# Kernel tuning notes

Hardware: AMD Instinct MI355X
Metric: run time of the kernel (lower is better)

## Reference

```python
import jax, jax.numpy as jnp
import numpy as np

D_MODEL = 1024
D_HEAD = 64

def setup_inputs() -> dict:
    key = jax.random.key(0)
    ks = jax.random.split(key, 7)
    s = 1.0 / np.sqrt(D_MODEL)
    x = jax.random.normal(ks[0], (4, 4096, D_MODEL), dtype=jnp.float32)
    Wq = jax.random.uniform(ks[1], (D_MODEL, D_HEAD), jnp.float32, -s, s)
    bq = jax.random.uniform(ks[2], (D_HEAD,), jnp.float32, -s, s)
    Wk = jax.random.uniform(ks[3], (D_MODEL, D_HEAD), jnp.float32, -s, s)
    bk = jax.random.uniform(ks[4], (D_HEAD,), jnp.float32, -s, s)
    Wv = jax.random.uniform(ks[5], (D_MODEL, D_HEAD), jnp.float32, -s, s)
    bv = jax.random.uniform(ks[6], (D_HEAD,), jnp.float32, -s, s)
    return {"x": x, "Wq": Wq, "bq": bq, "Wk": Wk, "bk": bk, "Wv": Wv, "bv": bv}

def reference(x, Wq, bq, Wk, bk, Wv, bv):
    # x: [b, s, d_model] -> Q,K,V: [b, s, d_head]
    Q = jnp.einsum('bsd,dh->bsh', x, Wq) + bq
    K = jnp.einsum('bsd,dh->bsh', x, Wk) + bk
    V = jnp.einsum('bsd,dh->bsh', x, Wv) + bv
    scale = 1.0 / jnp.sqrt(jnp.asarray(D_HEAD, x.dtype))
    scores = jnp.einsum('bqh,bkh->bqk', Q, K) * scale  # [b, s, s]
    attn = jax.nn.softmax(scores, axis=-1)
    return jnp.einsum('bqk,bkh->bqh', attn, V)  # [b, s, d_head]
```

## Files before the change

### kernel.cpp

```cpp
#include <hip/hip_runtime.h>

typedef __bf16 bf16x8 __attribute__((ext_vector_type(8)));
typedef __bf16 bf16x4 __attribute__((ext_vector_type(4)));
typedef float f32x4 __attribute__((ext_vector_type(4)));
typedef unsigned short u16x8 __attribute__((ext_vector_type(8)));

union FragU { u16x8 u; bf16x8 b; };
union PackU { bf16x4 v; unsigned long long q; };

__device__ __forceinline__ unsigned short bfbits(float f) {
  __bf16 h = (__bf16)f;
  union { __bf16 h; unsigned short s; } cv; cv.h = h;
  return cv.s;
}

#define MFMA16(a, b, c) __builtin_amdgcn_mfma_f32_16x16x32_bf16((a), (b), (c), 0, 0, 0)

#define QSCALE 0.18033688011112042f

__global__ __launch_bounds__(256) void wt_kernel(
    const float* __restrict__ Wq, const float* __restrict__ Wk, const float* __restrict__ Wv,
    unsigned short* __restrict__ WF)
{
  const int m = blockIdx.x >> 5;
  const int c = blockIdx.x & 31;
  const float* W = (m == 0) ? Wq : ((m == 1) ? Wk : Wv);
  const int t = threadIdx.x >> 6;
  const int lane = threadIdx.x & 63;
  const int l15 = lane & 15;
  const int g = lane >> 4;
  unsigned short* dst = WF + ((((size_t)m * 32 + c) * 4 + t) * 64 + lane) * 8;
#pragma unroll
  for (int e = 0; e < 8; ++e)
    dst[e] = bfbits(W[(size_t)(32 * c + 8 * g + e) * 64 + (16 * t + l15)]);
}

__global__ __launch_bounds__(256, 1) void proj_kernel(
    const float* __restrict__ x, const unsigned short* __restrict__ WF,
    const float* __restrict__ bq, const float* __restrict__ bk, const float* __restrict__ bv,
    unsigned short* __restrict__ Qb, unsigned short* __restrict__ KF,
    unsigned short* __restrict__ VF)
{
  const int tid = threadIdx.x;
  const int lane = tid & 63;
  const int wid = tid >> 6;
  const int l15 = lane & 15;
  const int g = lane >> 4;
  const int row0 = blockIdx.x * 64 + wid * 16;

  f32x4 accQ[4], accK[4], accV[4];
  const f32x4 zero = {0.f, 0.f, 0.f, 0.f};
#pragma unroll
  for (int i = 0; i < 4; ++i) { accQ[i] = zero; accK[i] = zero; accV[i] = zero; }

  const float* xrow = x + (size_t)(row0 + l15) * 1024;

  f32x4 xx0[4], xx1[4];
  bf16x8 wq[2][4], wk[2][4], wv[2][4];

#define PLDX(XB, C) { xx0[XB] = *(const f32x4*)(xrow + 32 * (C) + 8 * g); \
                      xx1[XB] = *(const f32x4*)(xrow + 32 * (C) + 8 * g + 4); }
#define PLDW(WS, C) { _Pragma("unroll") for (int t = 0; t < 4; ++t) { \
    wq[WS][t] = *(const bf16x8*)(WF + ((((size_t)0 * 32 + (C)) * 4 + t) * 64 + lane) * 8); \
    wk[WS][t] = *(const bf16x8*)(WF + ((((size_t)1 * 32 + (C)) * 4 + t) * 64 + lane) * 8); \
    wv[WS][t] = *(const bf16x8*)(WF + ((((size_t)2 * 32 + (C)) * 4 + t) * 64 + lane) * 8); } }
#define PHALF(XB, WS, CXN, CWN) { \
    FragU xf; \
    _Pragma("unroll") for (int i = 0; i < 4; ++i) { \
      xf.b[i] = (__bf16)xx0[XB][i]; xf.b[4 + i] = (__bf16)xx1[XB][i]; } \
    if ((CXN) < 32) PLDX(XB, CXN); \
    _Pragma("unroll") for (int t = 0; t < 4; ++t) { \
      accQ[t] = MFMA16(xf.b, wq[WS][t], accQ[t]); \
      accK[t] = MFMA16(xf.b, wk[WS][t], accK[t]); \
      accV[t] = MFMA16(wv[WS][t], xf.b, accV[t]); } \
    if ((CWN) < 32) PLDW(WS, CWN); }

  PLDX(0, 0) PLDX(1, 1) PLDX(2, 2) PLDX(3, 3)
  PLDW(0, 0) PLDW(1, 1)

#pragma unroll 1
  for (int c = 0; c < 32; c += 4) {
    PHALF(0, 0, c + 4, c + 2)
    PHALF(1, 1, c + 5, c + 3)
    PHALF(2, 0, c + 6, c + 4)
    PHALF(3, 1, c + 7, c + 5)
  }

  const int b = blockIdx.x >> 6;
  const int kt = blockIdx.x & 63;
  const int q0 = row0 & 4095;
  unsigned short* Qbase = Qb + (size_t)b * 4096 * 64;
#pragma unroll
  for (int t = 0; t < 4; ++t) {
    const int h = 16 * t + l15;
    const float bqv = bq[h];
#pragma unroll
    for (int r = 0; r < 4; ++r)
      Qbase[(size_t)(q0 + 4 * g + r) * 64 + h] = bfbits((accQ[t][r] + bqv) * QSCALE);
  }
  unsigned short* KFb = KF + ((size_t)b * 64 + kt) * 4096;
  unsigned short* VFb = VF + ((size_t)b * 64 + kt) * 4096;
#pragma unroll
  for (int t = 0; t < 4; ++t) {
    const int h = 16 * t + l15;
    const float bkv = bk[h];
#pragma unroll
    for (int r = 0; r < 4; ++r) {
      KFb[(size_t)((wid * 2 + (t >> 1)) * 64 + (t & 1) * 32 + (l15 >> 3) * 16 + 4 * g + r) * 8 +
          (l15 & 7)] = bfbits(accK[t][r] + bkv);
      const int hv = 16 * t + 4 * g + r;
      VFb[(size_t)((t * 2 + (wid >> 1)) * 64 + (wid & 1) * 32 + (l15 >> 3) * 16 + 4 * g + r) * 8 +
          (l15 & 7)] = bfbits(accV[t][r] + bv[hv]);
    }
  }
}

__global__ __launch_bounds__(256, 2) void flash_kernel(
    const unsigned short* __restrict__ Qb, const unsigned short* __restrict__ KF,
    const unsigned short* __restrict__ VF, float* __restrict__ out)
{
  __shared__ __align__(16) unsigned char lds[36864];
  const int tid = threadIdx.x;
  const int lane = tid & 63;
  const int w = tid >> 6;
  const int l15 = lane & 15;
  const int g = lane >> 4;
  const int bid = blockIdx.x;
  const int xcd = bid & 7;
  const int b = xcd >> 1;
  const int qt = (bid >> 3) * 2 + (xcd & 1);
  const int q0 = qt * 32;

  const unsigned short* Qp = Qb + (size_t)b * 4096 * 64;
  const unsigned short* KFb = KF + (size_t)b * 262144;
  const unsigned short* VFb = VF + (size_t)b * 262144;

  const bf16x8 qfA0 = *(const bf16x8*)(Qp + (size_t)(q0 + l15) * 64 + 8 * g);
  const bf16x8 qfA1 = *(const bf16x8*)(Qp + (size_t)(q0 + l15) * 64 + 32 + 8 * g);
  const bf16x8 qfB0 = *(const bf16x8*)(Qp + (size_t)(q0 + 16 + l15) * 64 + 8 * g);
  const bf16x8 qfB1 = *(const bf16x8*)(Qp + (size_t)(q0 + 16 + l15) * 64 + 32 + 8 * g);

  f32x4 O_A[4], O_B[4];
  const f32x4 zero = {0.f, 0.f, 0.f, 0.f};
#pragma unroll
  for (int i = 0; i < 4; ++i) { O_A[i] = zero; O_B[i] = zero; }
  float mA = -INFINITY, lA = 0.f, mB = -INFINITY, lB = 0.f;
  unsigned short* PwA = (unsigned short*)lds + (w * 2 + 0) * 1152;
  unsigned short* PwB = (unsigned short*)lds + (w * 2 + 1) * 1152;

#define SM_HALF(S, mvar, lvar, OA, PW) { \
  float mt = fmaxf(fmaxf(S[0][0], S[0][1]), fmaxf(S[0][2], S[0][3])); \
  _Pragma("unroll") for (int t = 1; t < 4; ++t) \
    _Pragma("unroll") for (int r = 0; r < 4; ++r) mt = fmaxf(mt, S[t][r]); \
  mt = fmaxf(mt, __shfl_xor(mt, 16)); \
  mt = fmaxf(mt, __shfl_xor(mt, 32)); \
  if (!__all(mt <= mvar + 8.0f)) { \
    const float mnew = fmaxf(mvar, mt); \
    const float alpha = __builtin_amdgcn_exp2f(mvar - mnew); \
    mvar = mnew; lvar *= alpha; \
    _Pragma("unroll") for (int r = 0; r < 4; ++r) { \
      const float ar = __shfl(alpha, 4 * g + r); \
      OA[0][r] *= ar; OA[1][r] *= ar; OA[2][r] *= ar; OA[3][r] *= ar; } \
  } \
  float ps = 0.f; \
  _Pragma("unroll") for (int t = 0; t < 4; ++t) { \
    const float p0 = __builtin_amdgcn_exp2f(S[t][0] - mvar); \
    const float p1 = __builtin_amdgcn_exp2f(S[t][1] - mvar); \
    const float p2 = __builtin_amdgcn_exp2f(S[t][2] - mvar); \
    const float p3 = __builtin_amdgcn_exp2f(S[t][3] - mvar); \
    ps += (p0 + p1) + (p2 + p3); \
    PackU pk_; pk_.v[0] = (__bf16)p0; pk_.v[1] = (__bf16)p1; \
    pk_.v[2] = (__bf16)p2; pk_.v[3] = (__bf16)p3; \
    *(unsigned long long*)((PW) + l15 * 72 + 16 * t + 4 * g) = pk_.q; } \
  ps += __shfl_xor(ps, 16); \
  ps += __shfl_xor(ps, 32); \
  lvar += ps; }

#pragma unroll 1
  for (int kt = w; kt < 64; kt += 4) {
    const unsigned short* Kt = KFb + kt * 4096;
    const unsigned short* Vt = VFb + kt * 4096;
    bf16x8 kf[8], vf[8];
#pragma unroll
    for (int j = 0; j < 8; ++j) kf[j] = *(const bf16x8*)(Kt + (j * 64 + lane) * 8);
#pragma unroll
    for (int j = 0; j < 8; ++j) vf[j] = *(const bf16x8*)(Vt + (j * 64 + lane) * 8);
    f32x4 S_A[4], S_B[4];
#pragma unroll
    for (int t = 0; t < 4; ++t) {
      S_A[t] = zero;
      S_A[t] = MFMA16(kf[2 * t], qfA0, S_A[t]);
      S_A[t] = MFMA16(kf[2 * t + 1], qfA1, S_A[t]);
      S_B[t] = zero;
      S_B[t] = MFMA16(kf[2 * t], qfB0, S_B[t]);
      S_B[t] = MFMA16(kf[2 * t + 1], qfB1, S_B[t]);
    }
    SM_HALF(S_A, mA, lA, O_A, PwA)
    SM_HALF(S_B, mB, lB, O_B, PwB)
#pragma unroll
    for (int s = 0; s < 2; ++s) {
      const bf16x8 paA = *(const bf16x8*)(PwA + l15 * 72 + 32 * s + 8 * g);
      const bf16x8 paB = *(const bf16x8*)(PwB + l15 * 72 + 32 * s + 8 * g);
#pragma unroll
      for (int nt = 0; nt < 4; ++nt) {
        O_A[nt] = MFMA16(paA, vf[2 * nt + s], O_A[nt]);
        O_B[nt] = MFMA16(paB, vf[2 * nt + s], O_B[nt]);
      }
    }
  }

  __syncthreads();
  float* O_l = (float*)lds;
  float* mlp = (float*)(lds + 34816);
#pragma unroll
  for (int nt = 0; nt < 4; ++nt)
#pragma unroll
    for (int r = 0; r < 4; ++r) {
      O_l[((w * 2 + 0) * 16 + 4 * g + r) * 68 + 16 * nt + l15] = O_A[nt][r];
      O_l[((w * 2 + 1) * 16 + 4 * g + r) * 68 + 16 * nt + l15] = O_B[nt][r];
    }
  if (g == 0) {
    mlp[((w * 2 + 0) * 16 + l15) * 2] = mA; mlp[((w * 2 + 0) * 16 + l15) * 2 + 1] = lA;
    mlp[((w * 2 + 1) * 16 + l15) * 2] = mB; mlp[((w * 2 + 1) * 16 + l15) * 2 + 1] = lB;
  }
  __syncthreads();

  const int q = tid >> 3;
  const int h0 = (tid & 7) * 8;
  const int qh = q >> 4, qr = q & 15;
  float M = -INFINITY;
#pragma unroll
  for (int s = 0; s < 4; ++s) M = fmaxf(M, mlp[((s * 2 + qh) * 16 + qr) * 2]);
  float L = 0.f;
  f32x4 a0 = zero, a1 = zero;
#pragma unroll
  for (int s = 0; s < 4; ++s) {
    const int rowi = (s * 2 + qh) * 16 + qr;
    const float wgt = __builtin_amdgcn_exp2f(mlp[rowi * 2] - M);
    L += wgt * mlp[rowi * 2 + 1];
    const f32x4 o0 = *(const f32x4*)&O_l[rowi * 68 + h0];
    const f32x4 o1 = *(const f32x4*)&O_l[rowi * 68 + h0 + 4];
#pragma unroll
    for (int i = 0; i < 4; ++i) { a0[i] += wgt * o0[i]; a1[i] += wgt * o1[i]; }
  }
  const float inv = 1.0f / L;
  float* ob = out + ((size_t)b * 4096 + qt * 32 + q) * 64 + h0;
  f32x4 r0 = {a0[0] * inv, a0[1] * inv, a0[2] * inv, a0[3] * inv};
  f32x4 r1 = {a1[0] * inv, a1[1] * inv, a1[2] * inv, a1[3] * inv};
  *(f32x4*)ob = r0;
  *(f32x4*)(ob + 4) = r1;
}

extern "C" void kernel_launch(void* const* d_in, const int* in_sizes, int n_in,
                              void* d_out, int out_size, void* d_ws, size_t ws_size,
                              hipStream_t stream) {
  const float* x  = (const float*)d_in[0];
  const float* Wq = (const float*)d_in[1];
  const float* bq = (const float*)d_in[2];
  const float* Wk = (const float*)d_in[3];
  const float* bk = (const float*)d_in[4];
  const float* Wv = (const float*)d_in[5];
  const float* bv = (const float*)d_in[6];

  char* ws = (char*)d_ws;
  unsigned short* WF = (unsigned short*)ws;
  unsigned short* Qb = (unsigned short*)(ws + (512u << 10));
  unsigned short* KF = (unsigned short*)(ws + (512u << 10) + (2u << 20));
  unsigned short* VF = (unsigned short*)(ws + (512u << 10) + (4u << 20));
  float* out = (float*)d_out;

  hipLaunchKernelGGL(wt_kernel,    dim3(96),  dim3(256), 0, stream, Wq, Wk, Wv, WF);
  hipLaunchKernelGGL(proj_kernel,  dim3(256), dim3(256), 0, stream, x, WF, bq, bk, bv, Qb, KF, VF);
  hipLaunchKernelGGL(flash_kernel, dim3(512), dim3(256), 0, stream, Qb, KF, VF, out);
}
```

Baseline: 61.34 us.

## Split projection K-dimension across waves with LDS reduction, quadruple grid

The projection kernel now gives each block 16 rows instead of 64, and its four waves each handle one quarter of the 1024-wide reduction dimension. Partial Q/K/V accumulators are reduced through shared memory, and three waves write out Q, K and V respectively. The grid grows from 256 to 1024 blocks to fill more CUs and hide memory latency better. In exchange it adds a 48KB LDS buffer, a barrier and a reduction step, and each block reloads all the weights for only 16 rows.

```diff
diff --git a/kernel.cpp b/kernel.cpp
--- a/kernel.cpp
+++ b/kernel.cpp
@@ -35,18 +35,19 @@
     dst[e] = bfbits(W[(size_t)(32 * c + 8 * g + e) * 64 + (16 * t + l15)]);
 }
 
-__global__ __launch_bounds__(256, 1) void proj_kernel(
+__global__ __launch_bounds__(256, 3) void proj_kernel(
     const float* __restrict__ x, const unsigned short* __restrict__ WF,
     const float* __restrict__ bq, const float* __restrict__ bk, const float* __restrict__ bv,
     unsigned short* __restrict__ Qb, unsigned short* __restrict__ KF,
     unsigned short* __restrict__ VF)
 {
+  __shared__ f32x4 part[4][3][4][64];
   const int tid = threadIdx.x;
   const int lane = tid & 63;
-  const int wid = tid >> 6;
+  const int w = tid >> 6;
   const int l15 = lane & 15;
   const int g = lane >> 4;
-  const int row0 = blockIdx.x * 64 + wid * 16;
+  const int row0 = blockIdx.x * 16;
 
   f32x4 accQ[4], accK[4], accV[4];
   const f32x4 zero = {0.f, 0.f, 0.f, 0.f};
@@ -68,49 +69,83 @@
     FragU xf; \
     _Pragma("unroll") for (int i = 0; i < 4; ++i) { \
       xf.b[i] = (__bf16)xx0[XB][i]; xf.b[4 + i] = (__bf16)xx1[XB][i]; } \
-    if ((CXN) < 32) PLDX(XB, CXN); \
+    if ((CXN) < cend) PLDX(XB, CXN); \
     _Pragma("unroll") for (int t = 0; t < 4; ++t) { \
       accQ[t] = MFMA16(xf.b, wq[WS][t], accQ[t]); \
       accK[t] = MFMA16(xf.b, wk[WS][t], accK[t]); \
       accV[t] = MFMA16(wv[WS][t], xf.b, accV[t]); } \
-    if ((CWN) < 32) PLDW(WS, CWN); }
-
-  PLDX(0, 0) PLDX(1, 1) PLDX(2, 2) PLDX(3, 3)
-  PLDW(0, 0) PLDW(1, 1)
+    if ((CWN) < cend) PLDW(WS, CWN); }
+
+  const int c0 = w * 8;
+  const int cend = c0 + 8;
+  PLDX(0, c0) PLDX(1, c0 + 1) PLDX(2, c0 + 2) PLDX(3, c0 + 3)
+  PLDW(0, c0) PLDW(1, c0 + 1)
 
 #pragma unroll 1
-  for (int c = 0; c < 32; c += 4) {
+  for (int c = c0; c < cend; c += 4) {
     PHALF(0, 0, c + 4, c + 2)
     PHALF(1, 1, c + 5, c + 3)
     PHALF(2, 0, c + 6, c + 4)
     PHALF(3, 1, c + 7, c + 5)
   }
 
-  const int b = blockIdx.x >> 6;
-  const int kt = blockIdx.x & 63;
+#pragma unroll
+  for (int t = 0; t < 4; ++t) {
+    part[w][0][t][lane] = accQ[t];
+    part[w][1][t][lane] = accK[t];
+    part[w][2][t][lane] = accV[t];
+  }
+  __syncthreads();
+  if (w == 3) return;
+
+  const int m = w;
+  f32x4 sum[4];
+#pragma unroll
+  for (int t = 0; t < 4; ++t) {
+    f32x4 s = part[0][m][t][lane];
+#pragma unroll
+    for (int ws = 1; ws < 4; ++ws) {
+      const f32x4 p = part[ws][m][t][lane];
+#pragma unroll
+      for (int i = 0; i < 4; ++i) s[i] += p[i];
+    }
+    sum[t] = s;
+  }
+
+  const int b = blockIdx.x >> 8;
   const int q0 = row0 & 4095;
-  unsigned short* Qbase = Qb + (size_t)b * 4096 * 64;
-#pragma unroll
-  for (int t = 0; t < 4; ++t) {
-    const int h = 16 * t + l15;
-    const float bqv = bq[h];
-#pragma unroll
-    for (int r = 0; r < 4; ++r)
-      Qbase[(size_t)(q0 + 4 * g + r) * 64 + h] = bfbits((accQ[t][r] + bqv) * QSCALE);
-  }
-  unsigned short* KFb = KF + ((size_t)b * 64 + kt) * 4096;
-  unsigned short* VFb = VF + ((size_t)b * 64 + kt) * 4096;
-#pragma unroll
-  for (int t = 0; t < 4; ++t) {
-    const int h = 16 * t + l15;
-    const float bkv = bk[h];
-#pragma unroll
-    for (int r = 0; r < 4; ++r) {
-      KFb[(size_t)((wid * 2 + (t >> 1)) * 64 + (t & 1) * 32 + (l15 >> 3) * 16 + 4 * g + r) * 8 +
-          (l15 & 7)] = bfbits(accK[t][r] + bkv);
-      const int hv = 16 * t + 4 * g + r;
-      VFb[(size_t)((t * 2 + (wid >> 1)) * 64 + (wid & 1) * 32 + (l15 >> 3) * 16 + 4 * g + r) * 8 +
-          (l15 & 7)] = bfbits(accV[t][r] + bv[hv]);
+  const int kt = (blockIdx.x & 255) >> 2;
+  const int r16 = blockIdx.x & 3;
+  if (m == 0) {
+    unsigned short* Qbase = Qb + (size_t)b * 4096 * 64;
+#pragma unroll
+    for (int t = 0; t < 4; ++t) {
+      const float bqv = bq[16 * t + l15];
+#pragma unroll
+      for (int r = 0; r < 4; ++r)
+        Qbase[(size_t)(q0 + 4 * g + r) * 64 + 16 * t + l15] =
+            bfbits((sum[t][r] + bqv) * QSCALE);
+    }
+  } else if (m == 1) {
+    unsigned short* KFb = KF + ((size_t)b * 64 + kt) * 4096;
+#pragma unroll
+    for (int t = 0; t < 4; ++t) {
+      const float bkv = bk[16 * t + l15];
+#pragma unroll
+      for (int r = 0; r < 4; ++r)
+        KFb[(size_t)((r16 * 2 + (t >> 1)) * 64 + (t & 1) * 32 + (l15 >> 3) * 16 + 4 * g + r) * 8 +
+            (l15 & 7)] = bfbits(sum[t][r] + bkv);
+    }
+  } else {
+    unsigned short* VFb = VF + ((size_t)b * 64 + kt) * 4096;
+#pragma unroll
+    for (int t = 0; t < 4; ++t) {
+#pragma unroll
+      for (int r = 0; r < 4; ++r) {
+        const int hv = 16 * t + 4 * g + r;
+        VFb[(size_t)((t * 2 + (r16 >> 1)) * 64 + (r16 & 1) * 32 + (l15 >> 3) * 16 + 4 * g + r) * 8 +
+            (l15 & 7)] = bfbits(sum[t][r] + bv[hv]);
+      }
     }
   }
 }
@@ -269,7 +304,7 @@
   unsigned short* VF = (unsigned short*)(ws + (512u << 10) + (4u << 20));
   float* out = (float*)d_out;
 
-  hipLaunchKernelGGL(wt_kernel,    dim3(96),  dim3(256), 0, stream, Wq, Wk, Wv, WF);
-  hipLaunchKernelGGL(proj_kernel,  dim3(256), dim3(256), 0, stream, x, WF, bq, bk, bv, Qb, KF, VF);
-  hipLaunchKernelGGL(flash_kernel, dim3(512), dim3(256), 0, stream, Qb, KF, VF, out);
-}
+  hipLaunchKernelGGL(wt_kernel,    dim3(96),   dim3(256), 0, stream, Wq, Wk, Wv, WF);
+  hipLaunchKernelGGL(proj_kernel,  dim3(1024), dim3(256), 0, stream, x, WF, bq, bk, bv, Qb, KF, VF);
+  hipLaunchKernelGGL(flash_kernel, dim3(512),  dim3(256), 0, stream, Qb, KF, VF, out);
+}
```

Result: slower. 85.88 us (+40.0%).

## Split QKV projection into separate per-matrix blocks for more parallelism

Applied to the files above, without the earlier changes.

The projection kernel now launches three times as many blocks. Each block computes only one of Q, K or V for its 64-row tile, with a single accumulator set and a smaller weight buffer. Launch bounds go from 1 to 4 blocks per SM, so more blocks run at once on the 256-CU device, where previously only 256 blocks ran. The cost is that x is read from memory three times instead of once, which adds traffic on a bandwidth-heavy kernel that reads 64MB of fp32 input.

```diff
diff --git a/kernel.cpp b/kernel.cpp
--- a/kernel.cpp
+++ b/kernel.cpp
@@ -35,82 +35,101 @@
     dst[e] = bfbits(W[(size_t)(32 * c + 8 * g + e) * 64 + (16 * t + l15)]);
 }
 
-__global__ __launch_bounds__(256, 1) void proj_kernel(
+__global__ __launch_bounds__(256, 4) void proj_kernel(
     const float* __restrict__ x, const unsigned short* __restrict__ WF,
     const float* __restrict__ bq, const float* __restrict__ bk, const float* __restrict__ bv,
     unsigned short* __restrict__ Qb, unsigned short* __restrict__ KF,
     unsigned short* __restrict__ VF)
 {
+  const int bid = blockIdx.x;
+  const int m = bid >> 8;
+  const int rb = bid & 255;
   const int tid = threadIdx.x;
   const int lane = tid & 63;
   const int wid = tid >> 6;
   const int l15 = lane & 15;
   const int g = lane >> 4;
-  const int row0 = blockIdx.x * 64 + wid * 16;
-
-  f32x4 accQ[4], accK[4], accV[4];
+  const int row0 = rb * 64 + wid * 16;
+
+  f32x4 acc[4];
   const f32x4 zero = {0.f, 0.f, 0.f, 0.f};
 #pragma unroll
-  for (int i = 0; i < 4; ++i) { accQ[i] = zero; accK[i] = zero; accV[i] = zero; }
+  for (int i = 0; i < 4; ++i) acc[i] = zero;
 
   const float* xrow = x + (size_t)(row0 + l15) * 1024;
+  const unsigned short* Wm = WF + (size_t)m * 65536;
 
   f32x4 xx0[4], xx1[4];
-  bf16x8 wq[2][4], wk[2][4], wv[2][4];
-
-#define PLDX(XB, C) { xx0[XB] = *(const f32x4*)(xrow + 32 * (C) + 8 * g); \
+  bf16x8 wf[2][4];
+
+#define QLDX(XB, C) { xx0[XB] = *(const f32x4*)(xrow + 32 * (C) + 8 * g); \
                       xx1[XB] = *(const f32x4*)(xrow + 32 * (C) + 8 * g + 4); }
-#define PLDW(WS, C) { _Pragma("unroll") for (int t = 0; t < 4; ++t) { \
-    wq[WS][t] = *(const bf16x8*)(WF + ((((size_t)0 * 32 + (C)) * 4 + t) * 64 + lane) * 8); \
-    wk[WS][t] = *(const bf16x8*)(WF + ((((size_t)1 * 32 + (C)) * 4 + t) * 64 + lane) * 8); \
-    wv[WS][t] = *(const bf16x8*)(WF + ((((size_t)2 * 32 + (C)) * 4 + t) * 64 + lane) * 8); } }
-#define PHALF(XB, WS, CXN, CWN) { \
+#define QLDW(WS, C) { _Pragma("unroll") for (int t = 0; t < 4; ++t) \
+    wf[WS][t] = *(const bf16x8*)(Wm + (((size_t)(C) * 4 + t) * 64 + lane) * 8); }
+#define QHALF(XB, WS, CXN, CWN, ISV) { \
     FragU xf; \
     _Pragma("unroll") for (int i = 0; i < 4; ++i) { \
       xf.b[i] = (__bf16)xx0[XB][i]; xf.b[4 + i] = (__bf16)xx1[XB][i]; } \
-    if ((CXN) < 32) PLDX(XB, CXN); \
+    if ((CXN) < 32) QLDX(XB, CXN); \
     _Pragma("unroll") for (int t = 0; t < 4; ++t) { \
-      accQ[t] = MFMA16(xf.b, wq[WS][t], accQ[t]); \
-      accK[t] = MFMA16(xf.b, wk[WS][t], accK[t]); \
-      accV[t] = MFMA16(wv[WS][t], xf.b, accV[t]); } \
-    if ((CWN) < 32) PLDW(WS, CWN); }
-
-  PLDX(0, 0) PLDX(1, 1) PLDX(2, 2) PLDX(3, 3)
-  PLDW(0, 0) PLDW(1, 1)
-
+      if (ISV) acc[t] = MFMA16(wf[WS][t], xf.b, acc[t]); \
+      else     acc[t] = MFMA16(xf.b, wf[WS][t], acc[t]); } \
+    if ((CWN) < 32) QLDW(WS, CWN); }
+
+  QLDX(0, 0) QLDX(1, 1) QLDX(2, 2) QLDX(3, 3)
+  QLDW(0, 0) QLDW(1, 1)
+
+  if (m == 2) {
 #pragma unroll 1
-  for (int c = 0; c < 32; c += 4) {
-    PHALF(0, 0, c + 4, c + 2)
-    PHALF(1, 1, c + 5, c + 3)
-    PHALF(2, 0, c + 6, c + 4)
-    PHALF(3, 1, c + 7, c + 5)
-  }
-
-  const int b = blockIdx.x >> 6;
-  const int kt = blockIdx.x & 63;
+    for (int c = 0; c < 32; c += 4) {
+      QHALF(0, 0, c + 4, c + 2, 1)
+      QHALF(1, 1, c + 5, c + 3, 1)
+      QHALF(2, 0, c + 6, c + 4, 1)
+      QHALF(3, 1, c + 7, c + 5, 1)
+    }
+  } else {
+#pragma unroll 1
+    for (int c = 0; c < 32; c += 4) {
+      QHALF(0, 0, c + 4, c + 2, 0)
+      QHALF(1, 1, c + 5, c + 3, 0)
+      QHALF(2, 0, c + 6, c + 4, 0)
+      QHALF(3, 1, c + 7, c + 5, 0)
+    }
+  }
+
+  const int b = rb >> 6;
+  const int kt = rb & 63;
   const int q0 = row0 & 4095;
-  unsigned short* Qbase = Qb + (size_t)b * 4096 * 64;
-#pragma unroll
-  for (int t = 0; t < 4; ++t) {
-    const int h = 16 * t + l15;
-    const float bqv = bq[h];
-#pragma unroll
-    for (int r = 0; r < 4; ++r)
-      Qbase[(size_t)(q0 + 4 * g + r) * 64 + h] = bfbits((accQ[t][r] + bqv) * QSCALE);
-  }
-  unsigned short* KFb = KF + ((size_t)b * 64 + kt) * 4096;
-  unsigned short* VFb = VF + ((size_t)b * 64 + kt) * 4096;
-#pragma unroll
-  for (int t = 0; t < 4; ++t) {
-    const int h = 16 * t + l15;
-    const float bkv = bk[h];
-#pragma unroll
-    for (int r = 0; r < 4; ++r) {
-      KFb[(size_t)((wid * 2 + (t >> 1)) * 64 + (t & 1) * 32 + (l15 >> 3) * 16 + 4 * g + r) * 8 +
-          (l15 & 7)] = bfbits(accK[t][r] + bkv);
-      const int hv = 16 * t + 4 * g + r;
-      VFb[(size_t)((t * 2 + (wid >> 1)) * 64 + (wid & 1) * 32 + (l15 >> 3) * 16 + 4 * g + r) * 8 +
-          (l15 & 7)] = bfbits(accV[t][r] + bv[hv]);
+  if (m == 0) {
+    unsigned short* Qbase = Qb + (size_t)b * 4096 * 64;
+#pragma unroll
+    for (int t = 0; t < 4; ++t) {
+      const float bqv = bq[16 * t + l15];
+#pragma unroll
+      for (int r = 0; r < 4; ++r)
+        Qbase[(size_t)(q0 + 4 * g + r) * 64 + 16 * t + l15] =
+            bfbits((acc[t][r] + bqv) * QSCALE);
+    }
+  } else if (m == 1) {
+    unsigned short* KFb = KF + ((size_t)b * 64 + kt) * 4096;
+#pragma unroll
+    for (int t = 0; t < 4; ++t) {
+      const float bkv = bk[16 * t + l15];
+#pragma unroll
+      for (int r = 0; r < 4; ++r)
+        KFb[(size_t)((wid * 2 + (t >> 1)) * 64 + (t & 1) * 32 + (l15 >> 3) * 16 + 4 * g + r) * 8 +
+            (l15 & 7)] = bfbits(acc[t][r] + bkv);
+    }
+  } else {
+    unsigned short* VFb = VF + ((size_t)b * 64 + kt) * 4096;
+#pragma unroll
+    for (int t = 0; t < 4; ++t) {
+#pragma unroll
+      for (int r = 0; r < 4; ++r) {
+        const int hv = 16 * t + 4 * g + r;
+        VFb[(size_t)((t * 2 + (wid >> 1)) * 64 + (wid & 1) * 32 + (l15 >> 3) * 16 + 4 * g + r) * 8 +
+            (l15 & 7)] = bfbits(acc[t][r] + bv[hv]);
+      }
     }
   }
 }
@@ -270,6 +289,6 @@
   float* out = (float*)d_out;
 
   hipLaunchKernelGGL(wt_kernel,    dim3(96),  dim3(256), 0, stream, Wq, Wk, Wv, WF);
-  hipLaunchKernelGGL(proj_kernel,  dim3(256), dim3(256), 0, stream, x, WF, bq, bk, bv, Qb, KF, VF);
+  hipLaunchKernelGGL(proj_kernel,  dim3(768), dim3(256), 0, stream, x, WF, bq, bk, bv, Qb, KF, VF);
   hipLaunchKernelGGL(flash_kernel, dim3(512), dim3(256), 0, stream, Qb, KF, VF, out);
 }
```

New measurement: 81.56 us. 33.0% more time.

## Stage x tiles through swizzled LDS with coalesced loads in projection kernel

Applied to the files above, without the earlier changes.

The projection kernel now loads x with fully coalesced 512-byte row segments per half-wave into registers, writes them into a double-buffered, XOR-swizzled per-wave LDS tile, and reads MFMA fragments back from LDS. Previously each lane loaded scattered 32-byte pieces of its row directly from global memory. This aims to improve global memory coalescing for the dominant x read. It adds LDS traffic, 64KB of shared memory per block, and register staging.

```diff
diff --git a/kernel.cpp b/kernel.cpp
--- a/kernel.cpp
+++ b/kernel.cpp
@@ -41,11 +41,14 @@
     unsigned short* __restrict__ Qb, unsigned short* __restrict__ KF,
     unsigned short* __restrict__ VF)
 {
+  __shared__ float ldsx[4][2][2048];
   const int tid = threadIdx.x;
   const int lane = tid & 63;
   const int wid = tid >> 6;
   const int l15 = lane & 15;
   const int g = lane >> 4;
+  const int h = lane >> 5;
+  const int u = lane & 31;
   const int row0 = blockIdx.x * 64 + wid * 16;
 
   f32x4 accQ[4], accK[4], accV[4];
@@ -53,37 +56,59 @@
 #pragma unroll
   for (int i = 0; i < 4; ++i) { accQ[i] = zero; accK[i] = zero; accV[i] = zero; }
 
-  const float* xrow = x + (size_t)(row0 + l15) * 1024;
-
-  f32x4 xx0[4], xx1[4];
+  const float* xbase = x + (size_t)(row0 + h) * 1024 + u * 4;
+
+  f32x4 st[8];
+  f32x4 xx[8];
   bf16x8 wq[2][4], wk[2][4], wv[2][4];
 
-#define PLDX(XB, C) { xx0[XB] = *(const f32x4*)(xrow + 32 * (C) + 8 * g); \
-                      xx1[XB] = *(const f32x4*)(xrow + 32 * (C) + 8 * g + 4); }
+#define STLD(CK) { _Pragma("unroll") for (int j = 0; j < 8; ++j) \
+    st[j] = *(const f32x4*)(xbase + (CK) * 128 + j * 2048); }
+
+#define STWR(P) { _Pragma("unroll") for (int j = 0; j < 8; ++j) { \
+    const int row_ = 2 * j + h; \
+    *(f32x4*)&ldsx[wid][P][row_ * 128 + ((u ^ (row_ & 7)) * 4)] = st[j]; } }
+
+#define LDSRD(P) { _Pragma("unroll") for (int cl = 0; cl < 4; ++cl) { \
+    const int u0_ = cl * 8 + 2 * g; \
+    const int k_ = l15 & 7; \
+    xx[2 * cl]     = *(const f32x4*)&ldsx[wid][P][l15 * 128 + ((u0_ ^ k_) * 4)]; \
+    xx[2 * cl + 1] = *(const f32x4*)&ldsx[wid][P][l15 * 128 + (((u0_ + 1) ^ k_) * 4)]; } }
+
 #define PLDW(WS, C) { _Pragma("unroll") for (int t = 0; t < 4; ++t) { \
     wq[WS][t] = *(const bf16x8*)(WF + ((((size_t)0 * 32 + (C)) * 4 + t) * 64 + lane) * 8); \
     wk[WS][t] = *(const bf16x8*)(WF + ((((size_t)1 * 32 + (C)) * 4 + t) * 64 + lane) * 8); \
     wv[WS][t] = *(const bf16x8*)(WF + ((((size_t)2 * 32 + (C)) * 4 + t) * 64 + lane) * 8); } }
-#define PHALF(XB, WS, CXN, CWN) { \
+
+#define PHALF(CL, WS, CWN) { \
     FragU xf; \
     _Pragma("unroll") for (int i = 0; i < 4; ++i) { \
-      xf.b[i] = (__bf16)xx0[XB][i]; xf.b[4 + i] = (__bf16)xx1[XB][i]; } \
-    if ((CXN) < 32) PLDX(XB, CXN); \
+      xf.b[i] = (__bf16)xx[2 * (CL)][i]; xf.b[4 + i] = (__bf16)xx[2 * (CL) + 1][i]; } \
     _Pragma("unroll") for (int t = 0; t < 4; ++t) { \
       accQ[t] = MFMA16(xf.b, wq[WS][t], accQ[t]); \
       accK[t] = MFMA16(xf.b, wk[WS][t], accK[t]); \
       accV[t] = MFMA16(wv[WS][t], xf.b, accV[t]); } \
     if ((CWN) < 32) PLDW(WS, CWN); }
 
-  PLDX(0, 0) PLDX(1, 1) PLDX(2, 2) PLDX(3, 3)
-  PLDW(0, 0) PLDW(1, 1)
+  STLD(0)
+  STWR(0)
+  STLD(1)
+  PLDW(0, 0)
+  PLDW(1, 1)
 
 #pragma unroll 1
-  for (int c = 0; c < 32; c += 4) {
-    PHALF(0, 0, c + 4, c + 2)
-    PHALF(1, 1, c + 5, c + 3)
-    PHALF(2, 0, c + 6, c + 4)
-    PHALF(3, 1, c + 7, c + 5)
+  for (int ck = 0; ck < 8; ++ck) {
+    const int p = ck & 1;
+    if (ck < 7) STWR(p ^ 1)
+    if (ck < 6) STLD(ck + 2)
+    LDSRD(p)
+    {
+      const int c = ck * 4;
+      PHALF(0, ((c + 0) & 1), c + 2)
+      PHALF(1, ((c + 1) & 1), c + 3)
+      PHALF(2, ((c + 2) & 1), c + 4)
+      PHALF(3, ((c + 3) & 1), c + 5)
+    }
   }
 
   const int b = blockIdx.x >> 6;
@@ -92,18 +117,18 @@
   unsigned short* Qbase = Qb + (size_t)b * 4096 * 64;
 #pragma unroll
   for (int t = 0; t < 4; ++t) {
-    const int h = 16 * t + l15;
-    const float bqv = bq[h];
+    const int hh = 16 * t + l15;
+    const float bqv = bq[hh];
 #pragma unroll
     for (int r = 0; r < 4; ++r)
-      Qbase[(size_t)(q0 + 4 * g + r) * 64 + h] = bfbits((accQ[t][r] + bqv) * QSCALE);
+      Qbase[(size_t)(q0 + 4 * g + r) * 64 + hh] = bfbits((accQ[t][r] + bqv) * QSCALE);
   }
   unsigned short* KFb = KF + ((size_t)b * 64 + kt) * 4096;
   unsigned short* VFb = VF + ((size_t)b * 64 + kt) * 4096;
 #pragma unroll
   for (int t = 0; t < 4; ++t) {
-    const int h = 16 * t + l15;
-    const float bkv = bk[h];
+    const int hh = 16 * t + l15;
+    const float bkv = bk[hh];
 #pragma unroll
     for (int r = 0; r < 4; ++r) {
       KFb[(size_t)((wid * 2 + (t >> 1)) * 64 + (t & 1) * 32 + (l15 >> 3) * 16 + 4 * g + r) * 8 +
```

After: 62.04 us. About the same (+1.1%).
